# Kernel tuning notes

Measured on AMD Instinct MI355X. Metric: run time of the kernel, lower is better.

The kernel has to match this reference:

```python
import jax, jax.numpy as jnp
import numpy as np

D_MODEL = 256
N_HEADS = 4
SPARSITY_RATIO = 0.5
B, N, E = 4, 2048, 65536


def setup_inputs() -> dict:
    key = jax.random.key(0)
    ks = jax.random.split(key, 16)
    d, h = D_MODEL, D_MODEL // 2
    s = 1.0 / np.sqrt(d)
    inp = {
        "x": jax.random.normal(ks[0], (B, N, d), dtype=jnp.float32),
        "edge_index": jax.random.randint(ks[1], (2, E), 0, N, dtype=jnp.int64),
        "Wq": jax.random.uniform(ks[2], (d, d), minval=-s, maxval=s),
        "bq": jnp.zeros((d,), jnp.float32),
        "Wk": jax.random.uniform(ks[3], (d, d), minval=-s, maxval=s),
        "bk": jnp.zeros((d,), jnp.float32),
        "Wv": jax.random.uniform(ks[4], (d, d), minval=-s, maxval=s),
        "bv": jnp.zeros((d,), jnp.float32),
        "Wo": jax.random.uniform(ks[5], (d, d), minval=-s, maxval=s),
        "bo": jnp.zeros((d,), jnp.float32),
        "Wg1": jax.random.uniform(ks[6], (d, h), minval=-s, maxval=s),  # gnn conv1 (in,out)
        "bg1": jnp.zeros((h,), jnp.float32),
        "Wg2": jax.random.uniform(ks[7], (h, 1), minval=-s, maxval=s),  # gnn conv2
        "bg2": jnp.zeros((1,), jnp.float32),
    }
    return inp


def reference(x, edge_index, Wq, bq, Wk, bk, Wv, bv, Wo, bo, Wg1, bg1, Wg2, bg2):
    b, n, d = x.shape
    hd = d // N_HEADS
    row, col = edge_index[0], edge_index[1]

    # Lightweight GNN topo scores, vmapped over batch (replaces python loop)
    def gnn(xb):
        aggr = jax.ops.segment_sum(xb[col], row, num_segments=n)  # [N, d]
        hdn = jax.nn.relu(aggr @ Wg1 + bg1)
        return (hdn @ Wg2 + bg2)[:, 0]  # [N]

    topo_scores = jax.vmap(gnn)(x)  # [B, N]

    Q = (x @ Wq + bq).reshape(b, n, N_HEADS, hd)
    K = (x @ Wk + bk).reshape(b, n, N_HEADS, hd)
    V = (x @ Wv + bv).reshape(b, n, N_HEADS, hd)

    content_scores = jnp.einsum('bnhd,bmhd->bhnm', Q, K) / np.sqrt(hd)
    content_attn = jax.nn.softmax(content_scores, axis=-1)  # [B,H,N,N]

    # Edge mask (identical across batch, assignment semantics => set)
    edge_mask = jnp.zeros((n, n), jnp.float32).at[row, col].set(1.0)

    # top-k columns per batch (same columns for every query row i)
    k = max(1, int(n * (1 - SPARSITY_RATIO)))
    _, topk_idx = jax.lax.top_k(topo_scores, k)  # [B, k]
    col_mask = jnp.zeros((b, n), jnp.float32).at[jnp.arange(b)[:, None], topk_idx].set(1.0)

    sparse_mask = jnp.maximum(edge_mask[None, :, :], col_mask[:, None, :])  # [B,N,N]
    mask4 = jnp.broadcast_to(sparse_mask[:, None, :, :], (b, N_HEADS, n, n))

    sparse_attn = content_attn * mask4
    sparse_attn = sparse_attn / (jnp.sum(sparse_attn, axis=-1, keepdims=True) + 1e-8)

    out = jnp.einsum('bhnm,bmhd->bnhd', sparse_attn, V).reshape(b, n, d)
    out = out @ Wo + bo
    return out, mask4
```

## Files before the change

kernel.cpp:

```cpp
#include <hip/hip_runtime.h>
#include <hip/hip_bf16.h>
#include <stdint.h>

#define NTOK 2048
#define NB 4
#define DM 256
#define HD 64
#define NE 65536
#define SCAP 128
#define NKSL 4

typedef __bf16 bf16x8 __attribute__((ext_vector_type(8)));
typedef float f32x4 __attribute__((ext_vector_type(4)));

#define MFMA16 __builtin_amdgcn_mfma_f32_16x16x32_bf16

__device__ __forceinline__ unsigned short f2bf(float f) {
    union { float f; uint32_t u; } v; v.f = f;
    return (unsigned short)((v.u + 0x7fffu + ((v.u >> 16) & 1u)) >> 16);
}

__global__ __launch_bounds__(256) void k_prep(const float* __restrict__ x,
                       unsigned short* __restrict__ xb,
                       const float* __restrict__ W0, const float* __restrict__ W1,
                       const float* __restrict__ W2, const float* __restrict__ W3,
                       unsigned short* __restrict__ WT, float4* __restrict__ wsz,
                       const float* __restrict__ Wg1, float* __restrict__ y) {
    __shared__ float xs[16][256];
    int bid = blockIdx.x, t = threadIdx.x;
    if (bid < 132) {
        wsz[bid * 256 + t] = float4{0.f, 0.f, 0.f, 0.f};
    } else if (bid < 1156) {
        int b2 = bid - 132;
        int sel = b2 >> 8;
        const float* W = sel == 0 ? W0 : sel == 1 ? W1 : sel == 2 ? W2 : W3;
        int e = (b2 & 255) * 256 + t;
        int n = e >> 8, k = e & 255;
        WT[sel * 65536 + e] = f2bf(W[k * 256 + n]);
    } else {
        int m0 = (bid - 1156) * 16;
        #pragma unroll
        for (int j = 0; j < 16; ++j) {
            float v = x[(size_t)(m0 + j) * DM + t];
            xs[j][t] = v;
            xb[(size_t)(m0 + j) * DM + t] = f2bf(v);
        }
        __syncthreads();
        int c = t & 127, g = t >> 7;
        float acc[8] = {0.f, 0.f, 0.f, 0.f, 0.f, 0.f, 0.f, 0.f};
        const float* xr = &xs[g * 8][0];
        #pragma unroll 4
        for (int r = 0; r < DM; ++r) {
            float w = Wg1[r * 128 + c];
            #pragma unroll
            for (int j = 0; j < 8; ++j) acc[j] += xr[j * 256 + r] * w;
        }
        #pragma unroll
        for (int j = 0; j < 8; ++j) y[(size_t)(m0 + g * 8 + j) * 128 + c] = acc[j];
    }
}

__global__ void k_edges(const int* __restrict__ ei, uint32_t* __restrict__ cursor,
                        uint32_t* __restrict__ scol, uint32_t* __restrict__ ebits) {
    int e = blockIdx.x * 256 + threadIdx.x;
    int r = ei[e];
    int c = ei[NE + e];
    uint32_t slot = atomicAdd(&cursor[r], 1u);
    if (slot < SCAP) scol[r * SCAP + slot] = (uint32_t)c;
    atomicOr(&ebits[r * 64 + (c >> 5)], 1u << (c & 31));
}

__global__ __launch_bounds__(256) void k_gnn_qkv(
    const float* __restrict__ y, const uint32_t* __restrict__ cursor,
    const uint32_t* __restrict__ scol,
    const float* __restrict__ bg1, const float* __restrict__ Wg2,
    const float* __restrict__ bg2, float* __restrict__ topo,
    const unsigned short* __restrict__ xbf, const unsigned short* __restrict__ WT,
    const float* __restrict__ bq, const float* __restrict__ bk, const float* __restrict__ bv,
    unsigned short* __restrict__ qo, unsigned short* __restrict__ kt,
    unsigned short* __restrict__ vt3) {
    int bid = blockIdx.x, t = threadIdx.x;
    if (bid < 2048) {
        int i = bid;
        int d = t & 127, bp = t >> 7;
        uint32_t cnt = cursor[i]; if (cnt > SCAP) cnt = SCAP;
        const uint32_t* sc = scol + i * SCAP;
        const float* yA = y + (size_t)(bp * NTOK) * 128 + d;
        const float* yB = y + (size_t)((bp + 2) * NTOK) * 128 + d;
        double A0 = 0, A1 = 0, A2 = 0, A3 = 0;
        double B0 = 0, B1 = 0, B2 = 0, B3 = 0;
        uint32_t e = 0;
        for (; e + 3 < cnt; e += 4) {
            int c0 = sc[e] << 7, c1 = sc[e + 1] << 7;
            int c2 = sc[e + 2] << 7, c3 = sc[e + 3] << 7;
            A0 += (double)yA[c0]; A1 += (double)yA[c1];
            A2 += (double)yA[c2]; A3 += (double)yA[c3];
            B0 += (double)yB[c0]; B1 += (double)yB[c1];
            B2 += (double)yB[c2]; B3 += (double)yB[c3];
        }
        for (; e < cnt; ++e) {
            int c0 = sc[e] << 7;
            A0 += (double)yA[c0];
            B0 += (double)yB[c0];
        }
        double hA = (A0 + A1) + (A2 + A3) + (double)bg1[d];
        double hB = (B0 + B1) + (B2 + B3) + (double)bg1[d];
        double w2 = (double)Wg2[d];
        double vA = (hA > 0 ? hA : 0.0) * w2;
        double vB = (hB > 0 ? hB : 0.0) * w2;
        #pragma unroll
        for (int s = 32; s >= 1; s >>= 1) {
            vA += __shfl_xor(vA, s);
            vB += __shfl_xor(vB, s);
        }
        __shared__ double red[4][2];
        int wid = t >> 6;
        if ((t & 63) == 0) { red[wid][0] = vA; red[wid][1] = vB; }
        __syncthreads();
        if (t == 0) {
            double bb = (double)bg2[0];
            topo[0 * NTOK + i] = (float)(red[0][0] + red[1][0] + bb);
            topo[2 * NTOK + i] = (float)(red[0][1] + red[1][1] + bb);
            topo[1 * NTOK + i] = (float)(red[2][0] + red[3][0] + bb);
            topo[3 * NTOK + i] = (float)(red[2][1] + red[3][1] + bb);
        }
    } else {
        int b2 = bid - 2048;
        int z = b2 >> 9, r2 = b2 & 511;
        const unsigned short* W = WT + z * 65536;
        const float* bias = z == 0 ? bq : z == 1 ? bk : bv;

        int lane = t & 63, w = t >> 6;
        int l15 = lane & 15, grp = lane >> 4;
        int mbase = (r2 & 127) * 64 + w * 16;
        int nbase = (r2 >> 7) * 64;
        f32x4 acc0 = {0,0,0,0}, acc1 = {0,0,0,0}, acc2 = {0,0,0,0}, acc3 = {0,0,0,0};
        const unsigned short* ap = xbf + (size_t)(mbase + l15) * DM + grp * 8;
        const unsigned short* bp2 = W + (size_t)(nbase + l15) * DM + grp * 8;
        #pragma unroll
        for (int k0 = 0; k0 < DM; k0 += 32) {
            bf16x8 af = *(const bf16x8*)(ap + k0);
            acc0 = MFMA16(af, *(const bf16x8*)(bp2 + k0), acc0, 0, 0, 0);
            acc1 = MFMA16(af, *(const bf16x8*)(bp2 + 16 * DM + k0), acc1, 0, 0, 0);
            acc2 = MFMA16(af, *(const bf16x8*)(bp2 + 32 * DM + k0), acc2, 0, 0, 0);
            acc3 = MFMA16(af, *(const bf16x8*)(bp2 + 48 * DM + k0), acc3, 0, 0, 0);
        }
        f32x4 accs[4] = {acc0, acc1, acc2, acc3};
        #pragma unroll
        for (int ct = 0; ct < 4; ++ct) {
            #pragma unroll
            for (int r = 0; r < 4; ++r) {
                int m = mbase + grp * 4 + r;
                int n = nbase + ct * 16 + l15;
                float v = accs[ct][r] + bias[n];
                if (z == 0) {
                    qo[(size_t)m * DM + n] = f2bf(v);
                } else {
                    int b = m >> 11, tok = m & 2047, h = n >> 6, d = n & 63;
                    int bh = (b << 2) + h;
                    if (z == 1) {
                        kt[(size_t)bh * 131072 + (tok >> 4) * 1024 + (tok & 15) * 64 + d] = f2bf(v);
                    } else {
                        vt3[(size_t)bh * 131072 + (tok >> 5) * 2048 + d * 32 + (tok & 31)] = f2bf(v);
                    }
                }
            }
        }
    }
}

__global__ __launch_bounds__(256) void k_topk(const float* __restrict__ topo,
                                              uint32_t* __restrict__ colbits) {
    int b = blockIdx.y, t = threadIdx.x;
    int i = blockIdx.x * 256 + t;
    __shared__ float4 sc4[NTOK / 4];
    const float4* tp = (const float4*)(topo + b * NTOK);
    for (int j = t; j < NTOK / 4; j += 256) sc4[j] = tp[j];
    __syncthreads();
    float si = ((const float*)sc4)[i];
    int rank = 0;
    #pragma unroll 2
    for (int jj = 0; jj < NTOK / 4; ++jj) {
        float4 v = sc4[jj];
        int j0 = jj * 4;
        rank += (v.x > si) || (v.x == si && (j0    ) < i);
        rank += (v.y > si) || (v.y == si && (j0 + 1) < i);
        rank += (v.z > si) || (v.z == si && (j0 + 2) < i);
        rank += (v.w > si) || (v.w == si && (j0 + 3) < i);
    }
    unsigned long long m = __ballot(rank < 1024);
    int lane = t & 63;
    if (lane == 0)       colbits[b * 64 + (i >> 5)] = (uint32_t)m;
    else if (lane == 32) colbits[b * 64 + (i >> 5)] = (uint32_t)(m >> 32);
}

__global__ __launch_bounds__(256) void k_attn_part(const unsigned short* __restrict__ Q,
                                                   const unsigned short* __restrict__ KT,
                                                   const unsigned short* __restrict__ VT3,
                                                   const uint32_t* __restrict__ ebits,
                                                   const uint32_t* __restrict__ colbits,
                                                   float* __restrict__ po,
                                                   float* __restrict__ pl) {
    __shared__ unsigned short ksh[2][2048];
    __shared__ unsigned short vsh[2][2048];
    int bid = blockIdx.x;
    int t = threadIdx.x;
    int lane = t & 63, w = t >> 6;
    int l15 = lane & 15, grp = lane >> 4;
    int ks = bid >> 9;
    int bh = (bid >> 5) & 15, b = bh >> 2, h = bh & 3;
    int q = (bid & 31) * 64 + w * 16 + l15;

    const unsigned short* qp = Q + (size_t)(b * NTOK + q) * DM + h * HD + grp * 8;
    bf16x8 qf0 = *(const bf16x8*)(qp);
    bf16x8 qf1 = *(const bf16x8*)(qp + 32);
    const unsigned short* Kt = KT + (size_t)bh * 131072;
    const unsigned short* Vt = VT3 + (size_t)bh * 131072;
    const uint32_t* eb = ebits + q * 64;
    const uint32_t* cbp = colbits + b * 64;

    int kb0 = ks * (NTOK / NKSL);

    int kso = (t * 16) ^ (((t >> 3) & 7) << 4);
    int vso = (t * 16) ^ (((t >> 2) & 7) << 4);
    int swz = (l15 & 7) << 4;

    {
        uint4 kv = *(const uint4*)(Kt + (size_t)(kb0 >> 4) * 1024 + t * 8);
        *(uint4*)((char*)&ksh[0][0] + kso) = kv;
        uint4 vv = *(const uint4*)(Vt + (size_t)(kb0 >> 5) * 2048 + t * 8);
        *(uint4*)((char*)&vsh[0][0] + vso) = vv;
    }
    __syncthreads();

    f32x4 o0 = {0,0,0,0}, o1 = {0,0,0,0}, o2 = {0,0,0,0}, o3 = {0,0,0,0};
    float psum = 0.f;

    for (int it = 0; it < NTOK / NKSL / 32; ++it) {
        int buf = it & 1;
        if (it + 1 < NTOK / NKSL / 32) {
            int kb = kb0 + (it + 1) * 32;
            uint4 kv = *(const uint4*)(Kt + (size_t)(kb >> 4) * 1024 + t * 8);
            *(uint4*)((char*)&ksh[buf ^ 1][0] + kso) = kv;
            uint4 vv = *(const uint4*)(Vt + (size_t)(kb >> 5) * 2048 + t * 8);
            *(uint4*)((char*)&vsh[buf ^ 1][0] + vso) = vv;
        }
        int kb = kb0 + it * 32;
        const char* kp = (const char*)&ksh[buf][0];
        const char* vp = (const char*)&vsh[buf][0];

        f32x4 st0 = {0,0,0,0}, st1 = {0,0,0,0};
        st0 = MFMA16(*(const bf16x8*)(kp + ((l15 * 128 + grp * 16) ^ swz)),        qf0, st0, 0, 0, 0);
        st0 = MFMA16(*(const bf16x8*)(kp + ((l15 * 128 + 64 + grp * 16) ^ swz)),   qf1, st0, 0, 0, 0);
        st1 = MFMA16(*(const bf16x8*)(kp + (((16 + l15) * 128 + grp * 16) ^ swz)), qf0, st1, 0, 0, 0);
        st1 = MFMA16(*(const bf16x8*)(kp + (((16 + l15) * 128 + 64 + grp * 16) ^ swz)), qf1, st1, 0, 0, 0);

        uint32_t mw = eb[kb >> 5] | cbp[kb >> 5];
        float p[8];
        #pragma unroll
        for (int r = 0; r < 4; ++r) {
            int p0 = grp * 4 + r;
            p[r]     = ((mw >> p0) & 1u)        ? __expf(st0[r] * 0.125f - 8.0f) : 0.f;
            p[4 + r] = ((mw >> (16 + p0)) & 1u) ? __expf(st1[r] * 0.125f - 8.0f) : 0.f;
        }
        #pragma unroll
        for (int j = 0; j < 8; ++j) psum += p[j];

        uint32_t pk00, pk01, pk10, pk11;
        asm("v_cvt_pk_bf16_f32 %0, %1, %2" : "=v"(pk00) : "v"(p[0]), "v"(p[1]));
        asm("v_cvt_pk_bf16_f32 %0, %1, %2" : "=v"(pk01) : "v"(p[2]), "v"(p[3]));
        asm("v_cvt_pk_bf16_f32 %0, %1, %2" : "=v"(pk10) : "v"(p[4]), "v"(p[5]));
        asm("v_cvt_pk_bf16_f32 %0, %1, %2" : "=v"(pk11) : "v"(p[6]), "v"(p[7]));
        union { uint32_t u[4]; bf16x8 v; } pf;
        #pragma unroll
        for (int wi = 0; wi < 4; ++wi) {
            int src = (((grp * 2 + (wi >> 1)) & 3) << 4) | l15;
            uint32_t lo = (uint32_t)__shfl((int)((wi & 1) ? pk01 : pk00), src);
            uint32_t hi = (uint32_t)__shfl((int)((wi & 1) ? pk11 : pk10), src);
            pf.u[wi] = (lane >= 32) ? hi : lo;
        }

        o0 = MFMA16(*(const bf16x8*)(vp + ((l15 * 64 + grp * 16) ^ swz)),          pf.v, o0, 0, 0, 0);
        o1 = MFMA16(*(const bf16x8*)(vp + (((16 + l15) * 64 + grp * 16) ^ swz)),   pf.v, o1, 0, 0, 0);
        o2 = MFMA16(*(const bf16x8*)(vp + (((32 + l15) * 64 + grp * 16) ^ swz)),   pf.v, o2, 0, 0, 0);
        o3 = MFMA16(*(const bf16x8*)(vp + (((48 + l15) * 64 + grp * 16) ^ swz)),   pf.v, o3, 0, 0, 0);
        __syncthreads();
    }
    psum += __shfl_xor(psum, 16);
    psum += __shfl_xor(psum, 32);

    float* pb = po + (((size_t)(ks * 16 + bh) * NTOK + q) * HD);
    *(f32x4*)(pb + 0 * 16 + grp * 4) = o0;
    *(f32x4*)(pb + 1 * 16 + grp * 4) = o1;
    *(f32x4*)(pb + 2 * 16 + grp * 4) = o2;
    *(f32x4*)(pb + 3 * 16 + grp * 4) = o3;
    if (grp == 0) pl[(size_t)(ks * 16 + bh) * NTOK + q] = psum;
}

__global__ __launch_bounds__(256) void k_fin(const float* __restrict__ po,
                                             const float* __restrict__ pl,
                                             unsigned short* __restrict__ aoutb) {
    const size_t SL = (size_t)16 * NTOK * HD;
    const size_t SLP = (size_t)16 * NTOK;
    int tid = blockIdx.x * 256 + threadIdx.x;
    int dc = tid & 7;
    int q = (tid >> 3) & 2047;
    int bh = tid >> 14;
    size_t rb = ((size_t)bh * NTOK + q) * HD + dc * 8;
    float4 s0 = *(const float4*)(po + rb);
    float4 s1 = *(const float4*)(po + rb + 4);
    #pragma unroll
    for (int ks = 1; ks < NKSL; ++ks) {
        float4 a = *(const float4*)(po + ks * SL + rb);
        float4 c = *(const float4*)(po + ks * SL + rb + 4);
        s0.x += a.x; s0.y += a.y; s0.z += a.z; s0.w += a.w;
        s1.x += c.x; s1.y += c.y; s1.z += c.z; s1.w += c.w;
    }
    float l = 0.f;
    #pragma unroll
    for (int ks = 0; ks < NKSL; ++ks) l += pl[ks * SLP + (size_t)bh * NTOK + q];
    float inv = 1.f / l;
    int b = bh >> 2, h = bh & 3;
    union { ushort4 u4[2]; uint4 v; } out;
    out.u4[0].x = f2bf(s0.x * inv); out.u4[0].y = f2bf(s0.y * inv);
    out.u4[0].z = f2bf(s0.z * inv); out.u4[0].w = f2bf(s0.w * inv);
    out.u4[1].x = f2bf(s1.x * inv); out.u4[1].y = f2bf(s1.y * inv);
    out.u4[1].z = f2bf(s1.z * inv); out.u4[1].w = f2bf(s1.w * inv);
    *(uint4*)(aoutb + ((size_t)(b * NTOK + q) * DM) + h * HD + dc * 8) = out.v;
}

__device__ __forceinline__ void mask_quad(int idx, const uint32_t* __restrict__ eb,
                                          const uint32_t* __restrict__ cb,
                                          float* __restrict__ mout) {
    int b = idx >> 19;
    int rem = idx & 524287;
    int i = rem >> 8;
    int j = (rem & 255) << 3;
    uint32_t mw = eb[i * 64 + (j >> 5)] | cb[b * 64 + (j >> 5)];
    int sh = j & 31;
    float4 v0, v1;
    v0.x = ((mw >> sh) & 1u) ? 1.f : 0.f;
    v0.y = ((mw >> (sh + 1)) & 1u) ? 1.f : 0.f;
    v0.z = ((mw >> (sh + 2)) & 1u) ? 1.f : 0.f;
    v0.w = ((mw >> (sh + 3)) & 1u) ? 1.f : 0.f;
    v1.x = ((mw >> (sh + 4)) & 1u) ? 1.f : 0.f;
    v1.y = ((mw >> (sh + 5)) & 1u) ? 1.f : 0.f;
    v1.z = ((mw >> (sh + 6)) & 1u) ? 1.f : 0.f;
    v1.w = ((mw >> (sh + 7)) & 1u) ? 1.f : 0.f;
    size_t base = (((size_t)b * 4) * NTOK + i) * NTOK + j;
    #pragma unroll
    for (int hh = 0; hh < 4; ++hh) {
        float* p = mout + base + (size_t)hh * NTOK * NTOK;
        *(float4*)p = v0;
        *(float4*)(p + 4) = v1;
    }
}

__global__ void k_mask4(const uint32_t* __restrict__ ebits, const uint32_t* __restrict__ colbits,
                        float* __restrict__ mout) {
    mask_quad(blockIdx.x * 256 + threadIdx.x, ebits, colbits, mout);
}

__global__ __launch_bounds__(256) void k_gemm_o(const unsigned short* __restrict__ A,
                                                const unsigned short* __restrict__ WT,
                                                const float* __restrict__ bias,
                                                float* __restrict__ out) {
    int bid = blockIdx.x;
    int lane = threadIdx.x & 63, w = threadIdx.x >> 6;
    int l15 = lane & 15, grp = lane >> 4;
    int mbase = (bid & 127) * 64 + w * 16;
    int nbase = (bid >> 7) * 64;
    f32x4 acc0 = {0,0,0,0}, acc1 = {0,0,0,0}, acc2 = {0,0,0,0}, acc3 = {0,0,0,0};
    const unsigned short* ap = A + (size_t)(mbase + l15) * DM + grp * 8;
    const unsigned short* bp = WT + (size_t)(nbase + l15) * DM + grp * 8;
    #pragma unroll
    for (int k0 = 0; k0 < DM; k0 += 32) {
        bf16x8 af = *(const bf16x8*)(ap + k0);
        acc0 = MFMA16(af, *(const bf16x8*)(bp + k0), acc0, 0, 0, 0);
        acc1 = MFMA16(af, *(const bf16x8*)(bp + 16 * DM + k0), acc1, 0, 0, 0);
        acc2 = MFMA16(af, *(const bf16x8*)(bp + 32 * DM + k0), acc2, 0, 0, 0);
        acc3 = MFMA16(af, *(const bf16x8*)(bp + 48 * DM + k0), acc3, 0, 0, 0);
    }
    f32x4 accs[4] = {acc0, acc1, acc2, acc3};
    #pragma unroll
    for (int ct = 0; ct < 4; ++ct) {
        #pragma unroll
        for (int r = 0; r < 4; ++r) {
            int m = mbase + grp * 4 + r;
            int n = nbase + ct * 16 + l15;
            out[(size_t)m * DM + n] = accs[ct][r] + bias[n];
        }
    }
}

extern "C" void kernel_launch(void* const* d_in, const int* in_sizes, int n_in,
                              void* d_out, int out_size, void* d_ws, size_t ws_size,
                              hipStream_t stream) {
    const float* x   = (const float*)d_in[0];
    const int*   ei  = (const int*)d_in[1];
    const float* Wq  = (const float*)d_in[2];
    const float* bq  = (const float*)d_in[3];
    const float* Wk  = (const float*)d_in[4];
    const float* bk  = (const float*)d_in[5];
    const float* Wv  = (const float*)d_in[6];
    const float* bv  = (const float*)d_in[7];
    const float* Wo  = (const float*)d_in[8];
    const float* bo  = (const float*)d_in[9];
    const float* Wg1 = (const float*)d_in[10];
    const float* bg1 = (const float*)d_in[11];
    const float* Wg2 = (const float*)d_in[12];
    const float* bg2 = (const float*)d_in[13];

    float* out0  = (float*)d_out;
    float* mask4 = out0 + (size_t)NB * NTOK * DM;

    uint8_t* big = (uint8_t*)mask4;
    unsigned short* qbf   = (unsigned short*)(big);
    unsigned short* kt    = (unsigned short*)(big + (4u  << 20));
    unsigned short* vt3   = (unsigned short*)(big + (8u  << 20));
    unsigned short* wt    = (unsigned short*)(big + (12u << 20));
    unsigned short* aoutb = (unsigned short*)(big + (12u << 20) + (512u << 10));
    uint32_t*       scol  = (uint32_t*)      (big + (16u << 20) + (512u << 10));
    unsigned short* xbf   = (unsigned short*)(big + (17u << 20) + (512u << 10));
    float*          y     = (float*)         (big + (21u << 20) + (512u << 10));
    float*          po    = (float*)         (big + (25u << 20) + (512u << 10));
    float*          pl    = (float*)         (big + (57u << 20) + (512u << 10));

    uint8_t* ws = (uint8_t*)d_ws;
    uint32_t* cursor  = (uint32_t*)(ws);
    uint32_t* ebits   = (uint32_t*)(ws + (16u << 10));
    uint32_t* colbits = (uint32_t*)(ws + (528u << 10));
    float*    topo    = (float*)(ws + (532u << 10));

    k_prep<<<1668, 256, 0, stream>>>(x, xbf, Wq, Wk, Wv, Wo, wt, (float4*)ws, Wg1, y);
    k_edges<<<256, 256, 0, stream>>>(ei, cursor, scol, ebits);
    k_gnn_qkv<<<3584, 256, 0, stream>>>(y, cursor, scol, bg1, Wg2, bg2, topo,
                                        xbf, wt, bq, bk, bv, qbf, kt, vt3);
    k_topk<<<dim3(8, 4), 256, 0, stream>>>(topo, colbits);
    k_attn_part<<<NKSL * 512, 256, 0, stream>>>(qbf, kt, vt3, ebits, colbits, po, pl);
    k_fin<<<1024, 256, 0, stream>>>(po, pl, aoutb);
    k_gemm_o<<<512, 256, 0, stream>>>(aoutb, wt + 196608, bo, out0);
    k_mask4<<<8192, 256, 0, stream>>>(ebits, colbits, mask4);
}
```

Before: 251.2 us.

## Split mask4 output writes across attention and output-GEMM kernels to overlap

The separate 256 MB mask-writing kernel is broken into row ranges. Most rows are written by extra blocks appended to the attention kernel, some by extra blocks appended to the output GEMM kernel, and the rest by a small trailing kernel. Intermediate buffers kept in the mask4 output region are moved so that each stage only overwrites mask rows whose scratch data is already dead. The aim is to hide the bandwidth-bound mask stores behind the compute-bound attention and GEMM work. The risk is that mask blocks compete with attention blocks for memory bandwidth and CU slots, and that the buffer aliasing offsets are fragile.

```diff
diff --git a/kernel.cpp b/kernel.cpp
--- a/kernel.cpp
+++ b/kernel.cpp
@@ -9,6 +9,8 @@
 #define NE 65536
 #define SCAP 128
 #define NKSL 4
+#define ROWS_A 2112
+#define ROWS_B 6272
 
 typedef __bf16 bf16x8 __attribute__((ext_vector_type(8)));
 typedef float f32x4 __attribute__((ext_vector_type(4)));
@@ -194,16 +196,44 @@
     else if (lane == 32) colbits[b * 64 + (i >> 5)] = (uint32_t)(m >> 32);
 }
 
-__global__ __launch_bounds__(256) void k_attn_part(const unsigned short* __restrict__ Q,
+__device__ __forceinline__ void mask_row(int rowidx, const uint32_t* __restrict__ eb,
+                                         const uint32_t* __restrict__ cb,
+                                         float* __restrict__ mout) {
+    int t = threadIdx.x;
+    int b = rowidx >> 13;
+    int i = rowidx & 2047;
+    int j0 = t << 3;
+    uint32_t mw = eb[i * 64 + (j0 >> 5)] | cb[b * 64 + (j0 >> 5)];
+    int sh = j0 & 31;
+    float4 v0, v1;
+    v0.x = ((mw >> sh) & 1u) ? 1.f : 0.f;
+    v0.y = ((mw >> (sh + 1)) & 1u) ? 1.f : 0.f;
+    v0.z = ((mw >> (sh + 2)) & 1u) ? 1.f : 0.f;
+    v0.w = ((mw >> (sh + 3)) & 1u) ? 1.f : 0.f;
+    v1.x = ((mw >> (sh + 4)) & 1u) ? 1.f : 0.f;
+    v1.y = ((mw >> (sh + 5)) & 1u) ? 1.f : 0.f;
+    v1.z = ((mw >> (sh + 6)) & 1u) ? 1.f : 0.f;
+    v1.w = ((mw >> (sh + 7)) & 1u) ? 1.f : 0.f;
+    float* p = mout + (size_t)rowidx * NTOK + j0;
+    *(float4*)p = v0;
+    *(float4*)(p + 4) = v1;
+}
+
+__global__ __launch_bounds__(256) void k_attn_mask(const unsigned short* __restrict__ Q,
                                                    const unsigned short* __restrict__ KT,
                                                    const unsigned short* __restrict__ VT3,
                                                    const uint32_t* __restrict__ ebits,
                                                    const uint32_t* __restrict__ colbits,
                                                    float* __restrict__ po,
-                                                   float* __restrict__ pl) {
+                                                   float* __restrict__ pl,
+                                                   float* __restrict__ mout) {
+    int bid = blockIdx.x;
+    if (bid >= 2048) {
+        mask_row(bid - 2048 + ROWS_B, ebits, colbits, mout);
+        return;
+    }
     __shared__ unsigned short ksh[2][2048];
     __shared__ unsigned short vsh[2][2048];
-    int bid = blockIdx.x;
     int t = threadIdx.x;
     int lane = t & 63, w = t >> 6;
     int l15 = lane & 15, grp = lane >> 4;
@@ -220,7 +250,6 @@
     const uint32_t* cbp = colbits + b * 64;
 
     int kb0 = ks * (NTOK / NKSL);
-
     int kso = (t * 16) ^ (((t >> 3) & 7) << 4);
     int vso = (t * 16) ^ (((t >> 2) & 7) << 4);
     int swz = (l15 & 7) << 4;
@@ -329,43 +358,10 @@
     *(uint4*)(aoutb + ((size_t)(b * NTOK + q) * DM) + h * HD + dc * 8) = out.v;
 }
 
-__device__ __forceinline__ void mask_quad(int idx, const uint32_t* __restrict__ eb,
-                                          const uint32_t* __restrict__ cb,
-                                          float* __restrict__ mout) {
-    int b = idx >> 19;
-    int rem = idx & 524287;
-    int i = rem >> 8;
-    int j = (rem & 255) << 3;
-    uint32_t mw = eb[i * 64 + (j >> 5)] | cb[b * 64 + (j >> 5)];
-    int sh = j & 31;
-    float4 v0, v1;
-    v0.x = ((mw >> sh) & 1u) ? 1.f : 0.f;
-    v0.y = ((mw >> (sh + 1)) & 1u) ? 1.f : 0.f;
-    v0.z = ((mw >> (sh + 2)) & 1u) ? 1.f : 0.f;
-    v0.w = ((mw >> (sh + 3)) & 1u) ? 1.f : 0.f;
-    v1.x = ((mw >> (sh + 4)) & 1u) ? 1.f : 0.f;
-    v1.y = ((mw >> (sh + 5)) & 1u) ? 1.f : 0.f;
-    v1.z = ((mw >> (sh + 6)) & 1u) ? 1.f : 0.f;
-    v1.w = ((mw >> (sh + 7)) & 1u) ? 1.f : 0.f;
-    size_t base = (((size_t)b * 4) * NTOK + i) * NTOK + j;
-    #pragma unroll
-    for (int hh = 0; hh < 4; ++hh) {
-        float* p = mout + base + (size_t)hh * NTOK * NTOK;
-        *(float4*)p = v0;
-        *(float4*)(p + 4) = v1;
-    }
-}
-
-__global__ void k_mask4(const uint32_t* __restrict__ ebits, const uint32_t* __restrict__ colbits,
-                        float* __restrict__ mout) {
-    mask_quad(blockIdx.x * 256 + threadIdx.x, ebits, colbits, mout);
-}
-
-__global__ __launch_bounds__(256) void k_gemm_o(const unsigned short* __restrict__ A,
-                                                const unsigned short* __restrict__ WT,
-                                                const float* __restrict__ bias,
-                                                float* __restrict__ out) {
-    int bid = blockIdx.x;
+__device__ __forceinline__ void gemm_o_body(int bid, const unsigned short* __restrict__ A,
+                                            const unsigned short* __restrict__ WT,
+                                            const float* __restrict__ bias,
+                                            float* __restrict__ out) {
     int lane = threadIdx.x & 63, w = threadIdx.x >> 6;
     int l15 = lane & 15, grp = lane >> 4;
     int mbase = (bid & 127) * 64 + w * 16;
@@ -391,6 +387,26 @@
             out[(size_t)m * DM + n] = accs[ct][r] + bias[n];
         }
     }
+}
+
+__global__ __launch_bounds__(256) void k_gemm_mask(const unsigned short* __restrict__ A,
+                                                   const unsigned short* __restrict__ WT,
+                                                   const float* __restrict__ bias,
+                                                   float* __restrict__ out,
+                                                   const uint32_t* __restrict__ ebits,
+                                                   const uint32_t* __restrict__ colbits,
+                                                   float* __restrict__ mout) {
+    int bid = blockIdx.x;
+    if (bid < 512) {
+        gemm_o_body(bid, A, WT, bias, out);
+    } else {
+        mask_row(bid - 512 + ROWS_A, ebits, colbits, mout);
+    }
+}
+
+__global__ void k_mask4b(const uint32_t* __restrict__ ebits, const uint32_t* __restrict__ colbits,
+                         float* __restrict__ mout) {
+    mask_row(blockIdx.x, ebits, colbits, mout);
 }
 
 extern "C" void kernel_launch(void* const* d_in, const int* in_sizes, int n_in,
@@ -420,11 +436,11 @@
     unsigned short* vt3   = (unsigned short*)(big + (8u  << 20));
     unsigned short* wt    = (unsigned short*)(big + (12u << 20));
     unsigned short* aoutb = (unsigned short*)(big + (12u << 20) + (512u << 10));
-    uint32_t*       scol  = (uint32_t*)      (big + (16u << 20) + (512u << 10));
-    unsigned short* xbf   = (unsigned short*)(big + (17u << 20) + (512u << 10));
-    float*          y     = (float*)         (big + (21u << 20) + (512u << 10));
-    float*          po    = (float*)         (big + (25u << 20) + (512u << 10));
-    float*          pl    = (float*)         (big + (57u << 20) + (512u << 10));
+    float*          po    = (float*)         (big + (16u << 20) + (512u << 10));
+    float*          pl    = (float*)         (big + (48u << 20) + (512u << 10));
+    unsigned short* xbf   = (unsigned short*)(big + (49u << 20));
+    uint32_t*       scol  = (uint32_t*)      (big + (53u << 20));
+    float*          y     = (float*)         (big + (54u << 20));
 
     uint8_t* ws = (uint8_t*)d_ws;
     uint32_t* cursor  = (uint32_t*)(ws);
@@ -437,8 +453,10 @@
     k_gnn_qkv<<<3584, 256, 0, stream>>>(y, cursor, scol, bg1, Wg2, bg2, topo,
                                         xbf, wt, bq, bk, bv, qbf, kt, vt3);
     k_topk<<<dim3(8, 4), 256, 0, stream>>>(topo, colbits);
-    k_attn_part<<<NKSL * 512, 256, 0, stream>>>(qbf, kt, vt3, ebits, colbits, po, pl);
+    k_attn_mask<<<2048 + (32768 - ROWS_B), 256, 0, stream>>>(qbf, kt, vt3, ebits, colbits,
+                                                             po, pl, mask4);
     k_fin<<<1024, 256, 0, stream>>>(po, pl, aoutb);
-    k_gemm_o<<<512, 256, 0, stream>>>(aoutb, wt + 196608, bo, out0);
-    k_mask4<<<8192, 256, 0, stream>>>(ebits, colbits, mask4);
-}
+    k_gemm_mask<<<512 + (ROWS_B - ROWS_A), 256, 0, stream>>>(aoutb, wt + 196608, bo, out0,
+                                                             ebits, colbits, mask4);
+    k_mask4b<<<ROWS_A, 256, 0, stream>>>(ebits, colbits, mask4);
+}
```

Result: faster. 242.5 us (median of 2 runs) (-3.5%).
